# Kernel optimization log

Measured on AMD Instinct MI355X. Metric: run time of the kernel, lower is better.

The kernel has to match this reference:

```python
import jax, jax.numpy as jnp
import numpy as np

N_E, N_C, N_DL, N_IT, N_EP, N_HA, N_CA, N_AS = 11964, 188, 100, 7, 100, 10, 10, 7
D = 128
B, S = 256, 400
N_V = N_E + 1      # hypergraph vertices (exercises)
N_HE = N_C + 1     # hyperedges (concepts)
MEMB = 3           # concept memberships per exercise
BN_EPS = 1e-5


def _hg_v2v_mean(X, pair_v, pair_e):
    # HGNN+ smoothing: vertex -> hyperedge (mean) -> vertex (mean)
    ones_e = jnp.ones(pair_e.shape, X.dtype)
    e_deg = jnp.clip(jax.ops.segment_sum(ones_e, pair_e, num_segments=N_HE), 1.0)
    v_deg = jnp.clip(jax.ops.segment_sum(ones_e, pair_v, num_segments=N_V), 1.0)
    E = jax.ops.segment_sum(X[pair_v], pair_e, num_segments=N_HE) / e_deg[:, None]
    return jax.ops.segment_sum(E[pair_e], pair_v, num_segments=N_V) / v_deg[:, None]


def _hgnnp_conv(X, W, b, gamma, beta, mean, var, pair_v, pair_e, is_last):
    X = X @ W + b
    X = (X - mean) * jax.lax.rsqrt(var + BN_EPS) * gamma + beta  # eval-mode BN
    X = _hg_v2v_mean(X, pair_v, pair_e)
    if not is_last:
        X = jax.nn.relu(X)
    return X


def setup_inputs() -> dict:
    key = jax.random.key(0)
    ks = jax.random.split(key, 32)
    inp = {}
    inp['input_e'] = jax.random.randint(ks[0], (B, S), 0, N_V)
    inp['input_ed'] = jax.random.randint(ks[1], (B, S), 0, N_DL + 1)
    inp['input_ep'] = jax.random.randint(ks[2], (B, S), 0, N_EP + 1)
    inp['input_a'] = jax.random.randint(ks[3], (B, S), 0, 2)
    inp['input_as'] = jax.random.randint(ks[4], (B, S), 0, N_AS + 1)
    inp['input_ha'] = jax.random.randint(ks[5], (B, S), 0, N_HA + 1)
    inp['input_ca'] = jax.random.randint(ks[6], (B, S), 0, N_CA + 1)
    inp['input_it'] = jax.random.randint(ks[7], (B, S), 0, N_IT + 1)
    inp['deliver_h'] = jnp.zeros((B, D), jnp.float32)
    # hypergraph incidence (exercise-concept Q-matrix edges)
    rng = np.random.default_rng(0)
    inp['pair_v'] = jnp.asarray(np.repeat(np.arange(N_V), MEMB))
    inp['pair_e'] = jnp.asarray(rng.integers(0, N_HE, size=N_V * MEMB))
    inp['ec_map'] = jax.random.randint(ks[8], (N_V,), 0, N_HE)
    inp['ecd_map'] = jax.random.randint(ks[9], (N_V,), 0, N_DL + 1)
    # embedding tables (xavier-ish scale)
    def emb(k, n):
        return jax.random.normal(k, (n, D), jnp.float32) * 0.05
    inp['e_table'] = emb(ks[10], N_V)
    inp['c_table'] = emb(ks[11], N_HE)
    inp['ed_table'] = emb(ks[12], N_DL + 1)
    inp['cd_table'] = emb(ks[13], N_DL + 1)
    inp['a_table'] = emb(ks[14], 2)
    inp['it_table'] = emb(ks[15], N_IT + 1)
    inp['ep_table'] = emb(ks[16], N_EP + 1)
    inp['ha_table'] = emb(ks[17], N_HA + 1)
    inp['ca_table'] = emb(ks[18], N_CA + 1)
    inp['as_table'] = emb(ks[19], N_AS + 1)
    # HGNNP conv 1 & 2
    def lin(k, din, dout):
        return jax.random.normal(k, (din, dout), jnp.float32) * (1.0 / np.sqrt(din))
    inp['W1'] = lin(ks[20], D, D); inp['b1'] = jnp.zeros((D,), jnp.float32)
    inp['g1'] = jnp.ones((D,), jnp.float32); inp['be1'] = jnp.zeros((D,), jnp.float32)
    inp['m1'] = jnp.zeros((D,), jnp.float32); inp['v1'] = jnp.ones((D,), jnp.float32)
    inp['W2'] = lin(ks[21], D, D); inp['b2'] = jnp.zeros((D,), jnp.float32)
    inp['g2'] = jnp.ones((D,), jnp.float32); inp['be2'] = jnp.zeros((D,), jnp.float32)
    inp['m2'] = jnp.zeros((D,), jnp.float32); inp['v2'] = jnp.ones((D,), jnp.float32)
    # linear_i: (d_e + d_dl + d_ep + d_c + d_dl) -> d_x
    inp['Wi'] = lin(ks[22], 5 * D, D); inp['bi'] = jnp.zeros((D,), jnp.float32)
    # GRU knowledge-state cell: input = concat(x, a_emb) -> 2D, hidden D, 3 gates
    inp['Wg'] = lin(ks[23], 2 * D, 3 * D)
    inp['Ug'] = lin(ks[24], D, 3 * D)
    inp['bg'] = jnp.zeros((3 * D,), jnp.float32)
    # linear_predicting_e: d_x -> 1
    inp['We'] = lin(ks[25], D, 1); inp['beo'] = jnp.zeros((1,), jnp.float32)
    # linear_predicting_s: 4*d -> 1
    inp['Ws'] = lin(ks[26], 4 * D, 1); inp['bs'] = jnp.zeros((1,), jnp.float32)
    return inp


def reference(input_e, input_ed, input_ep, input_a, input_as, input_ha, input_ca, input_it,
              deliver_h, pair_v, pair_e, ec_map, ecd_map,
              e_table, c_table, ed_table, cd_table, a_table, it_table, ep_table,
              ha_table, ca_table, as_table,
              W1, b1, g1, be1, m1, v1, W2, b2, g2, be2, m2, v2,
              Wi, bi, Wg, Ug, bg, We, beo, Ws, bs):
    # 2-layer HGNN+ over the exercise hypergraph
    X = _hgnnp_conv(e_table, W1, b1, g1, be1, m1, v1, pair_v, pair_e, is_last=False)
    X = _hgnnp_conv(X, W2, b2, g2, be2, m2, v2, pair_v, pair_e, is_last=True)
    # embedding gathers  [B,S,D]
    e_emb = X[input_e]
    c_emb = c_table[ec_map[input_e]]
    cd_emb = cd_table[ecd_map[input_e]]
    ed_emb = ed_table[input_ed]
    ep_emb = ep_table[input_ep]
    x = jnp.tanh(jnp.concatenate([e_emb, ed_emb, ep_emb, c_emb, cd_emb], -1) @ Wi + bi)  # [B,S,D]
    a_emb = a_table[input_a]
    xs = jnp.moveaxis(jnp.concatenate([x, a_emb], -1), 1, 0)  # [S,B,2D]
    xp = jnp.moveaxis(x, 1, 0)                                # [S,B,D]

    def step(h, inputs):
        xin, xq = inputs
        y = jax.nn.sigmoid((h * xq) @ We + beo)[..., 0]  # predict from prior knowledge state
        gi = xin @ Wg + bg
        gh = h @ Ug
        iz, ir, inn = jnp.split(gi, 3, -1)
        hz, hr, hn = jnp.split(gh, 3, -1)
        z = jax.nn.sigmoid(iz + hz)
        r = jax.nn.sigmoid(ir + hr)
        n = jnp.tanh(inn + r * hn)
        return (1.0 - z) * n + z * h, y

    _, ys = jax.lax.scan(step, deliver_h, (xs, xp))
    pred_main = jnp.moveaxis(ys, 0, 1)  # [B,S]
    s_in = jnp.concatenate([ha_table[input_ha], ca_table[input_ca],
                            as_table[input_as], it_table[input_it]], -1)
    pred_s = jax.nn.sigmoid(s_in @ Ws + bs)[..., 0]  # [B,S]
    return pred_s, pred_main
```

## Files before the change

### kernel.cpp

```cpp
#include <hip/hip_runtime.h>

#define N_V   11965
#define N_HE  189
#define NPAIR 35895
#define BB    256
#define SS    400
#define DD    128
#define BSR   102400

typedef __bf16 bf16x8 __attribute__((ext_vector_type(8)));
typedef float  f32x4  __attribute__((ext_vector_type(4)));

__device__ __forceinline__ ushort f2bf(float f) {
    unsigned x = __float_as_uint(f);
    return (ushort)((x + 0x7FFFu + ((x >> 16) & 1u)) >> 16);
}
__device__ __forceinline__ float bf2f(ushort u) { return __uint_as_float(((unsigned)u) << 16); }
__device__ __forceinline__ float sigm(float x) { return 1.f / (1.f + __expf(-x)); }
__device__ __forceinline__ float tanh_f(float x) { return 2.f * sigm(2.f * x) - 1.f; }

struct P1Args {
    const int* pair_e;
    const float *b1, *g1, *be1, *m1, *v1;
    const float *b2, *g2, *be2, *m2, *v2;
    const float *W1, *W2, *Wi, *Wg;
    const float *ed_t, *ep_t, *c_t, *cd_t, *a_t, *bi, *bg;
    const float *ha_t, *ca_t, *as_t, *it_t, *Ws;
    int* e_deg;
    float* aff;
    ushort *W1T, *W2T, *WiTe, *WgT;
    float *edW, *epW, *cW, *cdW, *agi, *sd;
};

__global__ __launch_bounds__(384) void p1_kernel(P1Args A) {
    int bid = blockIdx.x, t = threadIdx.x;
    if (bid == 0) {
        if (t < 128) {
            float s = A.g1[t] * rsqrtf(A.v1[t] + 1e-5f);
            A.aff[t] = s;
            A.aff[128 + t] = A.b1[t] * s + A.be1[t] - A.m1[t] * s;
        } else if (t < 256) {
            int d = t - 128;
            float s = A.g2[d] * rsqrtf(A.v2[d] + 1e-5f);
            A.aff[256 + d] = s;
            A.aff[384 + d] = A.b2[d] * s + A.be2[d] - A.m2[d] * s;
        }
        return;
    }
    bid -= 1;
    if (bid < 94) {
        int p = bid * 384 + t;
        if (p < NPAIR) atomicAdd(&A.e_deg[A.pair_e[p]], 1);
        return;
    }
    bid -= 94;
    if (bid < 43) {
        int i = bid * 384 + t;
        if (i < 16384) { int k = i >> 7, n = i & 127; A.W1T[n * 128 + k] = f2bf(A.W1[i]); }
        return;
    }
    bid -= 43;
    if (bid < 43) {
        int i = bid * 384 + t;
        if (i < 16384) { int k = i >> 7, n = i & 127; A.W2T[n * 128 + k] = f2bf(A.W2[i]); }
        return;
    }
    bid -= 43;
    if (bid < 43) {
        int i = bid * 384 + t;
        if (i < 16384) { int k = i >> 7, n = i & 127; A.WiTe[n * 128 + k] = f2bf(A.Wi[i]); }
        return;
    }
    bid -= 43;
    if (bid < 128) {
        int i = bid * 384 + t;
        if (i < 49152) { int k = i / 384, n = i % 384; A.WgT[n * 128 + k] = f2bf(A.Wg[i]); }
        return;
    }
    bid -= 128;
    if (bid < 101) {
        if (t < 128) {
            float acc = 0.f;
            for (int k = 0; k < 128; ++k)
                acc += A.ed_t[bid * 128 + k] * A.Wi[(128 + k) * 128 + t];
            A.edW[bid * 128 + t] = acc + A.bi[t];
        }
        return;
    }
    bid -= 101;
    if (bid < 101) {
        if (t < 128) {
            float acc = 0.f;
            for (int k = 0; k < 128; ++k)
                acc += A.ep_t[bid * 128 + k] * A.Wi[(256 + k) * 128 + t];
            A.epW[bid * 128 + t] = acc;
        }
        return;
    }
    bid -= 101;
    if (bid < 189) {
        if (t < 128) {
            float acc = 0.f;
            for (int k = 0; k < 128; ++k)
                acc += A.c_t[bid * 128 + k] * A.Wi[(384 + k) * 128 + t];
            A.cW[bid * 128 + t] = acc;
        }
        return;
    }
    bid -= 189;
    if (bid < 101) {
        if (t < 128) {
            float acc = 0.f;
            for (int k = 0; k < 128; ++k)
                acc += A.cd_t[bid * 128 + k] * A.Wi[(512 + k) * 128 + t];
            A.cdW[bid * 128 + t] = acc;
        }
        return;
    }
    bid -= 101;
    if (bid < 2) {
        float acc = 0.f;
        for (int k = 0; k < 128; ++k)
            acc += A.a_t[bid * 128 + k] * A.Wg[(128 + k) * 384 + t];
        A.agi[bid * 384 + t] = acc + A.bg[t];
        return;
    }
    bid -= 2;
    {
        int r = bid;
        const float* tab; int woff, row;
        if (r < 11)      { tab = A.ha_t; row = r;      woff = 0;   }
        else if (r < 22) { tab = A.ca_t; row = r - 11; woff = 128; }
        else if (r < 30) { tab = A.as_t; row = r - 22; woff = 256; }
        else             { tab = A.it_t; row = r - 30; woff = 384; }
        if (t < 64) {
            float p = tab[row * 128 + t] * A.Ws[woff + t]
                    + tab[row * 128 + 64 + t] * A.Ws[woff + 64 + t];
            #pragma unroll
            for (int o = 32; o > 0; o >>= 1) p += __shfl_xor(p, o);
            if (t == 0) A.sd[r] = p;
        }
    }
}

__global__ void cvt_kernel(const float* __restrict__ src, ushort* __restrict__ dst, int n) {
    int i = blockIdx.x * 256 + threadIdx.x;
    if (i < n) dst[i] = f2bf(src[i]);
}

__global__ void csr_prefix(const int* __restrict__ e_deg, int* __restrict__ start) {
    __shared__ int sc[256];
    int t = threadIdx.x;
    int d = (t < N_HE) ? e_deg[t] : 0;
    sc[t] = d;
    __syncthreads();
    for (int off = 1; off < 256; off <<= 1) {
        int v = (t >= off) ? sc[t - off] : 0;
        __syncthreads();
        sc[t] += v;
        __syncthreads();
    }
    if (t < N_HE) start[t] = sc[t] - d;
    if (t == N_HE - 1) start[N_HE] = sc[t];
}

__global__ void csr_fill(const int* __restrict__ pair_e, const int* __restrict__ pair_v,
                         const int* __restrict__ start, int* __restrict__ cursor,
                         int* __restrict__ list) {
    int p = blockIdx.x * 384 + threadIdx.x;
    if (p >= NPAIR) return;
    int e = pair_e[p];
    int pos = atomicAdd(&cursor[e], 1);
    list[start[e] + pos] = pair_v[p];
}

template <int NT>
__global__ __launch_bounds__(256) void gemm_mfma(
    const ushort* __restrict__ Amat, const ushort* __restrict__ BT,
    float* __restrict__ out, int M,
    const float* __restrict__ colS, const float* __restrict__ colB,
    const float* __restrict__ agi, const int* __restrict__ aidx) {
    const int N = NT * 16;
    int lane = threadIdx.x & 63, wave = threadIdx.x >> 6;
    int q = lane >> 4, c = lane & 15;
    int rowbase = blockIdx.x * 64 + wave * 16;
    int arow = rowbase + c;
    if (arow > M - 1) arow = M - 1;
    f32x4 acc[NT];
#pragma unroll
    for (int i = 0; i < NT; ++i) acc[i] = (f32x4){0.f, 0.f, 0.f, 0.f};
#pragma unroll
    for (int ko = 0; ko < 4; ++ko) {
        bf16x8 af = *(const bf16x8*)(Amat + (size_t)arow * 128 + ko * 32 + q * 8);
#pragma unroll
        for (int nt = 0; nt < NT; ++nt) {
            bf16x8 bfr = *(const bf16x8*)(BT + (size_t)(nt * 16 + c) * 128 + ko * 32 + q * 8);
            acc[nt] = __builtin_amdgcn_mfma_f32_16x16x32_bf16(af, bfr, acc[nt], 0, 0, 0);
        }
    }
#pragma unroll
    for (int nt = 0; nt < NT; ++nt) {
        int col = nt * 16 + c;
        float s = colS ? colS[col] : 1.f;
        float bb = colB ? colB[col] : 0.f;
#pragma unroll
        for (int r = 0; r < 4; ++r) {
            int row = rowbase + q * 4 + r;
            if (row < M) {
                float v = acc[nt][r] * s + bb;
                if (agi) v += agi[aidx[row] * N + col];
                out[(size_t)row * N + col] = v;
            }
        }
    }
}

__global__ __launch_bounds__(512) void edge_mean(const float* __restrict__ Y,
                                                 const int* __restrict__ list,
                                                 const int* __restrict__ start,
                                                 float* __restrict__ E) {
    __shared__ float red[4][128];
    int e = blockIdx.x;
    int d = threadIdx.x & 127, g = threadIdx.x >> 7;
    int s0 = start[e], n = start[e + 1] - s0;
    float acc = 0.f;
    for (int i = g; i < n; i += 4) acc += Y[(size_t)list[s0 + i] * DD + d];
    red[g][d] = acc;
    __syncthreads();
    if (g == 0) {
        float v = red[0][d] + red[1][d] + red[2][d] + red[3][d];
        E[e * DD + d] = v / (float)(n > 0 ? n : 1);
    }
}

__global__ void v_mean(const float* __restrict__ E, const int* __restrict__ pair_e,
                       ushort* __restrict__ Xo, int relu) {
    int idx = blockIdx.x * 256 + threadIdx.x;
    if (idx >= N_V * DD) return;
    int v = idx >> 7, d = idx & 127;
    float a = E[pair_e[3 * v] * DD + d] + E[pair_e[3 * v + 1] * DD + d] +
              E[pair_e[3 * v + 2] * DD + d];
    a *= (1.f / 3.f);
    if (relu) a = fmaxf(a, 0.f);
    Xo[idx] = f2bf(a);
}

__global__ void k3_kernel(const int* __restrict__ in_e, const int* __restrict__ in_ed,
                          const int* __restrict__ in_ep, const float* __restrict__ XW,
                          const float* __restrict__ cW, const float* __restrict__ cdW,
                          const float* __restrict__ edW, const float* __restrict__ epW,
                          const int* __restrict__ ec_map, const int* __restrict__ ecd_map,
                          ushort* __restrict__ xbf) {
    int idx = blockIdx.x * 256 + threadIdx.x;
    if (idx >= BSR * DD) return;
    int row = idx >> 7, d = idx & 127;
    int e = in_e[row];
    float v = XW[(size_t)e * DD + d] + cW[ec_map[e] * DD + d] + cdW[ecd_map[e] * DD + d] +
              edW[in_ed[row] * DD + d] + epW[in_ep[row] * DD + d];
    xbf[idx] = f2bf(tanh_f(v));
}

__global__ void pred_s_kernel(const int* __restrict__ ha, const int* __restrict__ ca,
                              const int* __restrict__ as_, const int* __restrict__ it,
                              const float* __restrict__ sd, const float* __restrict__ bs,
                              float* __restrict__ out) {
    int i = blockIdx.x * 256 + threadIdx.x;
    if (i >= BSR) return;
    float v = sd[ha[i]] + sd[11 + ca[i]] + sd[22 + as_[i]] + sd[30 + it[i]] + bs[0];
    out[i] = sigm(v);
}

__global__ void
__attribute__((amdgpu_flat_work_group_size(768, 768), amdgpu_waves_per_eu(3, 3)))
gru_scan(
    const float* __restrict__ gi, const ushort* __restrict__ xb,
    const float* __restrict__ Ug, const float* __restrict__ h0,
    const float* __restrict__ We, const float* __restrict__ beo_p,
    float* __restrict__ out) {
    __shared__ __align__(16) float h_s[128];
    __shared__ float pp1[384];
    __shared__ float pp0h[128];
    __shared__ float n_sL[128];
    __shared__ float p_s[128];
    int b = blockIdx.x, t = threadIdx.x;
    int khalf = (t >= 384) ? 1 : 0;
    int n = t - 384 * khalf;
    float ugf[64];
    {
        const float* up = Ug + (size_t)(khalf * 64) * 384 + n;
#pragma unroll
        for (int j = 0; j < 64; ++j) ugf[j] = up[j * 384];
    }
#pragma unroll
    for (int j = 0; j < 64; ++j) asm volatile("" : "+v"(ugf[j]));
    float beo = beo_p[0];
    float wev = 0.f;
    if (t < 128) { wev = We[t]; h_s[t] = h0[b * 128 + t]; }
    const float* gip = gi + (size_t)b * SS * 384;
    const ushort* xp = xb + (size_t)b * SS * 128;
    float gz_nx = 0.f, gr_nx = 0.f, gn_nx = 0.f, xw_nx = 0.f;
    if (t < 128) {
        gz_nx = gip[t];
        xw_nx = bf2f(xp[t]) * wev;
    } else if (t >= 256 && t < 384) {
        gr_nx = gip[t - 128];
        gn_nx = gip[t];
    }
    float* omain = out + BSR + b * SS;
    __syncthreads();
    for (int s = 0; s < SS; ++s) {
        float gz = gz_nx, gr = gr_nx, gn = gn_nx, xw = xw_nx;
        if (s + 1 < SS) {
            const float* g2 = gip + (size_t)(s + 1) * 384;
            if (t < 128) {
                gz_nx = g2[t];
                xw_nx = bf2f(xp[(size_t)(s + 1) * 128 + t]) * wev;
            } else if (t >= 256 && t < 384) {
                gr_nx = g2[t - 128];
                gn_nx = g2[t];
            }
        }
        const float4* h4 = (const float4*)h_s + khalf * 16;
        float4 a4 = make_float4(0.f, 0.f, 0.f, 0.f);
#pragma unroll
        for (int j = 0; j < 16; ++j) {
            float4 hv = h4[j];
            a4.x = fmaf(hv.x, ugf[4 * j + 0], a4.x);
            a4.y = fmaf(hv.y, ugf[4 * j + 1], a4.y);
            a4.z = fmaf(hv.z, ugf[4 * j + 2], a4.z);
            a4.w = fmaf(hv.w, ugf[4 * j + 3], a4.w);
        }
        float part = (a4.x + a4.y) + (a4.z + a4.w);
        if (khalf) pp1[n] = part;
        else if (t >= 128 && t < 256) pp0h[t - 128] = part;
        __syncthreads();
        float z = 0.f, h_old = 0.f;
        if (t < 128) {
            float gh = part + pp1[t];
            z = sigm(gz + gh);
            h_old = h_s[t];
            p_s[t] = h_old * xw;
        } else if (t >= 256 && t < 384) {
            float ghn = part + pp1[t];
            float ghr = pp0h[t - 256] + pp1[t - 128];
            float r = sigm(gr + ghr);
            n_sL[t - 256] = tanh_f(gn + r * ghn);
        }
        __syncthreads();
        if (t < 128) {
            h_s[t] = (1.f - z) * n_sL[t] + z * h_old;
        } else if (t >= 384 && t < 448) {
            int l = t - 384;
            float pv = p_s[l] + p_s[l + 64];
#pragma unroll
            for (int o = 32; o > 0; o >>= 1) pv += __shfl_xor(pv, o);
            if (l == 0) omain[s] = sigm(pv + beo);
        }
        __syncthreads();
    }
}

extern "C" void kernel_launch(void* const* d_in, const int* in_sizes, int n_in,
                              void* d_out, int out_size, void* d_ws, size_t ws_size,
                              hipStream_t stream) {
    const int* in_e   = (const int*)d_in[0];
    const int* in_ed  = (const int*)d_in[1];
    const int* in_ep  = (const int*)d_in[2];
    const int* in_a   = (const int*)d_in[3];
    const int* in_as  = (const int*)d_in[4];
    const int* in_ha  = (const int*)d_in[5];
    const int* in_ca  = (const int*)d_in[6];
    const int* in_it  = (const int*)d_in[7];
    const float* deliver_h = (const float*)d_in[8];
    const int* pair_v = (const int*)d_in[9];
    const int* pair_e = (const int*)d_in[10];
    const int* ec_map = (const int*)d_in[11];
    const int* ecd_map= (const int*)d_in[12];
    const float* e_table  = (const float*)d_in[13];
    const float* c_table  = (const float*)d_in[14];
    const float* ed_table = (const float*)d_in[15];
    const float* cd_table = (const float*)d_in[16];
    const float* a_table  = (const float*)d_in[17];
    const float* it_table = (const float*)d_in[18];
    const float* ep_table = (const float*)d_in[19];
    const float* ha_table = (const float*)d_in[20];
    const float* ca_table = (const float*)d_in[21];
    const float* as_table = (const float*)d_in[22];
    const float* W1 = (const float*)d_in[23];
    const float* b1 = (const float*)d_in[24];
    const float* g1 = (const float*)d_in[25];
    const float* be1= (const float*)d_in[26];
    const float* m1 = (const float*)d_in[27];
    const float* v1 = (const float*)d_in[28];
    const float* W2 = (const float*)d_in[29];
    const float* b2 = (const float*)d_in[30];
    const float* g2 = (const float*)d_in[31];
    const float* be2= (const float*)d_in[32];
    const float* m2 = (const float*)d_in[33];
    const float* v2 = (const float*)d_in[34];
    const float* Wi = (const float*)d_in[35];
    const float* bi = (const float*)d_in[36];
    const float* Wg = (const float*)d_in[37];
    const float* Ug = (const float*)d_in[38];
    const float* bg = (const float*)d_in[39];
    const float* We = (const float*)d_in[40];
    const float* beo= (const float*)d_in[41];
    const float* Ws = (const float*)d_in[42];
    const float* bs = (const float*)d_in[43];
    float* out = (float*)d_out;
    char* ws = (char*)d_ws;

    size_t off = 0;
    auto alloc = [&](size_t bytes) { size_t o = off; off += (bytes + 255) & ~(size_t)255; return o; };
    size_t o_degcur = alloc(378 * 4);
    size_t o_start  = alloc(190 * 4);
    size_t o_list   = alloc((size_t)NPAIR * 4);
    size_t o_aff    = alloc(512 * 4);
    size_t o_W1T    = alloc(16384 * 2);
    size_t o_W2T    = alloc(16384 * 2);
    size_t o_WiTe   = alloc(16384 * 2);
    size_t o_WgT    = alloc(49152 * 2);
    size_t o_edW    = alloc(101 * 128 * 4);
    size_t o_epW    = alloc(101 * 128 * 4);
    size_t o_cW     = alloc(189 * 128 * 4);
    size_t o_cdW    = alloc(101 * 128 * 4);
    size_t o_agi    = alloc(2 * 384 * 4);
    size_t o_sd     = alloc(38 * 4);
    size_t o_etb    = alloc((size_t)N_V * DD * 2);
    size_t o_E      = alloc((size_t)N_HE * DD * 4);
    size_t o_Y      = alloc((size_t)N_V * DD * 4);
    size_t o_X1     = alloc((size_t)N_V * DD * 2);
    size_t o_X2     = alloc((size_t)N_V * DD * 2);
    size_t o_XW     = alloc((size_t)N_V * DD * 4);
    size_t o_xbf    = alloc((size_t)BSR * DD * 2);
    size_t o_gi     = alloc((size_t)BSR * 384 * 4);

    int*    e_deg  = (int*)(ws + o_degcur);
    int*    cursor = e_deg + 189;
    int*    startp = (int*)(ws + o_start);
    int*    listp  = (int*)(ws + o_list);
    float*  aff    = (float*)(ws + o_aff);
    ushort* W1T    = (ushort*)(ws + o_W1T);
    ushort* W2T    = (ushort*)(ws + o_W2T);
    ushort* WiTe   = (ushort*)(ws + o_WiTe);
    ushort* WgT    = (ushort*)(ws + o_WgT);
    float*  edW    = (float*)(ws + o_edW);
    float*  epW    = (float*)(ws + o_epW);
    float*  cW     = (float*)(ws + o_cW);
    float*  cdW    = (float*)(ws + o_cdW);
    float*  agi    = (float*)(ws + o_agi);
    float*  sd     = (float*)(ws + o_sd);
    ushort* e_tb   = (ushort*)(ws + o_etb);
    float*  E      = (float*)(ws + o_E);
    float*  Y      = (float*)(ws + o_Y);
    ushort* X1b    = (ushort*)(ws + o_X1);
    ushort* X2b    = (ushort*)(ws + o_X2);
    float*  XW     = (float*)(ws + o_XW);
    ushort* xbf    = (ushort*)(ws + o_xbf);
    float*  gi     = (float*)(ws + o_gi);

    hipMemsetAsync(ws + o_degcur, 0, 378 * 4, stream);

    P1Args pa;
    pa.pair_e = pair_e;
    pa.b1 = b1; pa.g1 = g1; pa.be1 = be1; pa.m1 = m1; pa.v1 = v1;
    pa.b2 = b2; pa.g2 = g2; pa.be2 = be2; pa.m2 = m2; pa.v2 = v2;
    pa.W1 = W1; pa.W2 = W2; pa.Wi = Wi; pa.Wg = Wg;
    pa.ed_t = ed_table; pa.ep_t = ep_table; pa.c_t = c_table; pa.cd_t = cd_table;
    pa.a_t = a_table; pa.bi = bi; pa.bg = bg;
    pa.ha_t = ha_table; pa.ca_t = ca_table; pa.as_t = as_table; pa.it_t = it_table; pa.Ws = Ws;
    pa.e_deg = e_deg; pa.aff = aff;
    pa.W1T = W1T; pa.W2T = W2T; pa.WiTe = WiTe; pa.WgT = WgT;
    pa.edW = edW; pa.epW = epW; pa.cW = cW; pa.cdW = cdW; pa.agi = agi; pa.sd = sd;
    p1_kernel<<<884, 384, 0, stream>>>(pa);

    cvt_kernel<<<(N_V * DD + 255) / 256, 256, 0, stream>>>(e_table, e_tb, N_V * DD);
    csr_prefix<<<1, 256, 0, stream>>>(e_deg, startp);
    csr_fill<<<94, 384, 0, stream>>>(pair_e, pair_v, startp, cursor, listp);

    pred_s_kernel<<<(BSR + 255) / 256, 256, 0, stream>>>(in_ha, in_ca, in_as, in_it, sd, bs, out);

    gemm_mfma<8><<<(N_V + 63) / 64, 256, 0, stream>>>(e_tb, W1T, Y, N_V, aff, aff + 128,
                                                      nullptr, nullptr);
    edge_mean<<<N_HE, 512, 0, stream>>>(Y, listp, startp, E);
    v_mean<<<(N_V * DD + 255) / 256, 256, 0, stream>>>(E, pair_e, X1b, 1);
    gemm_mfma<8><<<(N_V + 63) / 64, 256, 0, stream>>>(X1b, W2T, Y, N_V, aff + 256, aff + 384,
                                                      nullptr, nullptr);
    edge_mean<<<N_HE, 512, 0, stream>>>(Y, listp, startp, E);
    v_mean<<<(N_V * DD + 255) / 256, 256, 0, stream>>>(E, pair_e, X2b, 0);
    gemm_mfma<8><<<(N_V + 63) / 64, 256, 0, stream>>>(X2b, WiTe, XW, N_V, nullptr, nullptr,
                                                      nullptr, nullptr);
    k3_kernel<<<(BSR * DD + 255) / 256, 256, 0, stream>>>(in_e, in_ed, in_ep, XW, cW, cdW, edW,
                                                          epW, ec_map, ecd_map, xbf);
    gemm_mfma<24><<<BSR / 64, 256, 0, stream>>>(xbf, WgT, gi, BSR, nullptr, nullptr, agi, in_a);
    gru_scan<<<BB, 768, 0, stream>>>(gi, xbf, Ug, deliver_h, We, beo, out);
}
```

Measured before the change: 1.015 ms.

## Store GRU recurrent weights as packed bf16 registers and split K four ways

The recurrent matrix Ug is now converted to a transposed bf16 copy in the prep kernel. Each GRU-scan thread holds 32 packed registers covering two output columns over a quarter of K, where it previously held 64 fp32 registers for one column over half of K. Partial sums go to a 4x392 shared buffer and are reduced by the gate threads. This lowers register pressure and relaxes the waves-per-EU bound. The cost is bf16 rounding of Ug inside the recurrence, extra unpack work and more shared-memory reads in the reduction.

After: 1.011 ms. About the same (-0.4%).

```diff
diff --git a/kernel.cpp b/kernel.cpp
--- a/kernel.cpp
+++ b/kernel.cpp
@@ -18,17 +18,19 @@
 __device__ __forceinline__ float bf2f(ushort u) { return __uint_as_float(((unsigned)u) << 16); }
 __device__ __forceinline__ float sigm(float x) { return 1.f / (1.f + __expf(-x)); }
 __device__ __forceinline__ float tanh_f(float x) { return 2.f * sigm(2.f * x) - 1.f; }
+__device__ __forceinline__ float blo(unsigned u) { return __uint_as_float(u << 16); }
+__device__ __forceinline__ float bhi(unsigned u) { return __uint_as_float(u); }
 
 struct P1Args {
     const int* pair_e;
     const float *b1, *g1, *be1, *m1, *v1;
     const float *b2, *g2, *be2, *m2, *v2;
-    const float *W1, *W2, *Wi, *Wg;
+    const float *W1, *W2, *Wi, *Wg, *Ug;
     const float *ed_t, *ep_t, *c_t, *cd_t, *a_t, *bi, *bg;
     const float *ha_t, *ca_t, *as_t, *it_t, *Ws;
     int* e_deg;
     float* aff;
-    ushort *W1T, *W2T, *WiTe, *WgT;
+    ushort *W1T, *W2T, *WiTe, *WgT, *UgT;
     float *edW, *epW, *cW, *cdW, *agi, *sd;
 };
 
@@ -75,6 +77,12 @@
     if (bid < 128) {
         int i = bid * 384 + t;
         if (i < 49152) { int k = i / 384, n = i % 384; A.WgT[n * 128 + k] = f2bf(A.Wg[i]); }
+        return;
+    }
+    bid -= 128;
+    if (bid < 128) {
+        int i = bid * 384 + t;
+        if (i < 49152) { int k = i / 384, n = i % 384; A.UgT[n * 128 + k] = f2bf(A.Ug[i]); }
         return;
     }
     bid -= 128;
@@ -271,28 +279,27 @@
 }
 
 __global__ void
-__attribute__((amdgpu_flat_work_group_size(768, 768), amdgpu_waves_per_eu(3, 3)))
+__attribute__((amdgpu_flat_work_group_size(768, 768), amdgpu_waves_per_eu(2, 3)))
 gru_scan(
     const float* __restrict__ gi, const ushort* __restrict__ xb,
-    const float* __restrict__ Ug, const float* __restrict__ h0,
+    const ushort* __restrict__ UgT, const float* __restrict__ h0,
     const float* __restrict__ We, const float* __restrict__ beo_p,
     float* __restrict__ out) {
     __shared__ __align__(16) float h_s[128];
-    __shared__ float pp1[384];
-    __shared__ float pp0h[128];
+    __shared__ float pp[4][392];
     __shared__ float n_sL[128];
     __shared__ float p_s[128];
     int b = blockIdx.x, t = threadIdx.x;
-    int khalf = (t >= 384) ? 1 : 0;
-    int n = t - 384 * khalf;
-    float ugf[64];
-    {
-        const float* up = Ug + (size_t)(khalf * 64) * 384 + n;
-#pragma unroll
-        for (int j = 0; j < 64; ++j) ugf[j] = up[j * 384];
-    }
-#pragma unroll
-    for (int j = 0; j < 64; ++j) asm volatile("" : "+v"(ugf[j]));
+    int kq = t / 192;
+    int cp = t % 192;
+    const unsigned* WA = (const unsigned*)(UgT + (size_t)cp * 128 + kq * 32);
+    const unsigned* WB = (const unsigned*)(UgT + (size_t)(cp + 192) * 128 + kq * 32);
+    unsigned a0 = WA[0], a1 = WA[1], a2 = WA[2], a3 = WA[3], a4 = WA[4], a5 = WA[5],
+             a6 = WA[6], a7 = WA[7], a8 = WA[8], a9 = WA[9], a10 = WA[10], a11 = WA[11],
+             a12 = WA[12], a13 = WA[13], a14 = WA[14], a15 = WA[15];
+    unsigned c0 = WB[0], c1 = WB[1], c2 = WB[2], c3 = WB[3], c4 = WB[4], c5 = WB[5],
+             c6 = WB[6], c7 = WB[7], c8 = WB[8], c9 = WB[9], c10 = WB[10], c11 = WB[11],
+             c12 = WB[12], c13 = WB[13], c14 = WB[14], c15 = WB[15];
     float beo = beo_p[0];
     float wev = 0.f;
     if (t < 128) { wev = We[t]; h_s[t] = h0[b * 128 + t]; }
@@ -309,6 +316,12 @@
     float* omain = out + BSR + b * SS;
     __syncthreads();
     for (int s = 0; s < SS; ++s) {
+#define PIN(X) asm volatile("" : "+v"(X));
+        PIN(a0) PIN(a1) PIN(a2) PIN(a3) PIN(a4) PIN(a5) PIN(a6) PIN(a7)
+        PIN(a8) PIN(a9) PIN(a10) PIN(a11) PIN(a12) PIN(a13) PIN(a14) PIN(a15)
+        PIN(c0) PIN(c1) PIN(c2) PIN(c3) PIN(c4) PIN(c5) PIN(c6) PIN(c7)
+        PIN(c8) PIN(c9) PIN(c10) PIN(c11) PIN(c12) PIN(c13) PIN(c14) PIN(c15)
+#undef PIN
         float gz = gz_nx, gr = gr_nx, gn = gn_nx, xw = xw_nx;
         if (s + 1 < SS) {
             const float* g2 = gip + (size_t)(s + 1) * 384;
@@ -320,31 +333,33 @@
                 gn_nx = g2[t];
             }
         }
-        const float4* h4 = (const float4*)h_s + khalf * 16;
-        float4 a4 = make_float4(0.f, 0.f, 0.f, 0.f);
-#pragma unroll
-        for (int j = 0; j < 16; ++j) {
-            float4 hv = h4[j];
-            a4.x = fmaf(hv.x, ugf[4 * j + 0], a4.x);
-            a4.y = fmaf(hv.y, ugf[4 * j + 1], a4.y);
-            a4.z = fmaf(hv.z, ugf[4 * j + 2], a4.z);
-            a4.w = fmaf(hv.w, ugf[4 * j + 3], a4.w);
-        }
-        float part = (a4.x + a4.y) + (a4.z + a4.w);
-        if (khalf) pp1[n] = part;
-        else if (t >= 128 && t < 256) pp0h[t - 128] = part;
+        const float4* h4 = (const float4*)h_s + kq * 8;
+        float accA = 0.f, accB = 0.f;
+#define FB(I, UL, UH, VL, VH) { float4 hv = h4[I]; \
+        accA = fmaf(hv.x, blo(UL), accA); accA = fmaf(hv.y, bhi(UL), accA); \
+        accA = fmaf(hv.z, blo(UH), accA); accA = fmaf(hv.w, bhi(UH), accA); \
+        accB = fmaf(hv.x, blo(VL), accB); accB = fmaf(hv.y, bhi(VL), accB); \
+        accB = fmaf(hv.z, blo(VH), accB); accB = fmaf(hv.w, bhi(VH), accB); }
+        FB(0, a0, a1, c0, c1)    FB(1, a2, a3, c2, c3)
+        FB(2, a4, a5, c4, c5)    FB(3, a6, a7, c6, c7)
+        FB(4, a8, a9, c8, c9)    FB(5, a10, a11, c10, c11)
+        FB(6, a12, a13, c12, c13) FB(7, a14, a15, c14, c15)
+#undef FB
+        pp[kq][cp] = accA;
+        pp[kq][cp + 192] = accB;
         __syncthreads();
         float z = 0.f, h_old = 0.f;
         if (t < 128) {
-            float gh = part + pp1[t];
-            z = sigm(gz + gh);
+            float S = pp[0][t] + pp[1][t] + pp[2][t] + pp[3][t];
+            z = sigm(gz + S);
             h_old = h_s[t];
             p_s[t] = h_old * xw;
         } else if (t >= 256 && t < 384) {
-            float ghn = part + pp1[t];
-            float ghr = pp0h[t - 256] + pp1[t - 128];
-            float r = sigm(gr + ghr);
-            n_sL[t - 256] = tanh_f(gn + r * ghn);
+            int j = t - 256;
+            float Sr = pp[0][128 + j] + pp[1][128 + j] + pp[2][128 + j] + pp[3][128 + j];
+            float Sn = pp[0][256 + j] + pp[1][256 + j] + pp[2][256 + j] + pp[3][256 + j];
+            float r = sigm(gr + Sr);
+            n_sL[j] = tanh_f(gn + r * Sn);
         }
         __syncthreads();
         if (t < 128) {
@@ -420,6 +435,7 @@
     size_t o_W2T    = alloc(16384 * 2);
     size_t o_WiTe   = alloc(16384 * 2);
     size_t o_WgT    = alloc(49152 * 2);
+    size_t o_UgT    = alloc(49152 * 2);
     size_t o_edW    = alloc(101 * 128 * 4);
     size_t o_epW    = alloc(101 * 128 * 4);
     size_t o_cW     = alloc(189 * 128 * 4);
@@ -444,6 +460,7 @@
     ushort* W2T    = (ushort*)(ws + o_W2T);
     ushort* WiTe   = (ushort*)(ws + o_WiTe);
     ushort* WgT    = (ushort*)(ws + o_WgT);
+    ushort* UgTp   = (ushort*)(ws + o_UgT);
     float*  edW    = (float*)(ws + o_edW);
     float*  epW    = (float*)(ws + o_epW);
     float*  cW     = (float*)(ws + o_cW);
@@ -465,14 +482,14 @@
     pa.pair_e = pair_e;
     pa.b1 = b1; pa.g1 = g1; pa.be1 = be1; pa.m1 = m1; pa.v1 = v1;
     pa.b2 = b2; pa.g2 = g2; pa.be2 = be2; pa.m2 = m2; pa.v2 = v2;
-    pa.W1 = W1; pa.W2 = W2; pa.Wi = Wi; pa.Wg = Wg;
+    pa.W1 = W1; pa.W2 = W2; pa.Wi = Wi; pa.Wg = Wg; pa.Ug = Ug;
     pa.ed_t = ed_table; pa.ep_t = ep_table; pa.c_t = c_table; pa.cd_t = cd_table;
     pa.a_t = a_table; pa.bi = bi; pa.bg = bg;
     pa.ha_t = ha_table; pa.ca_t = ca_table; pa.as_t = as_table; pa.it_t = it_table; pa.Ws = Ws;
     pa.e_deg = e_deg; pa.aff = aff;
-    pa.W1T = W1T; pa.W2T = W2T; pa.WiTe = WiTe; pa.WgT = WgT;
+    pa.W1T = W1T; pa.W2T = W2T; pa.WiTe = WiTe; pa.WgT = WgT; pa.UgT = UgTp;
     pa.edW = edW; pa.epW = epW; pa.cW = cW; pa.cdW = cdW; pa.agi = agi; pa.sd = sd;
-    p1_kernel<<<884, 384, 0, stream>>>(pa);
+    p1_kernel<<<1012, 384, 0, stream>>>(pa);
 
     cvt_kernel<<<(N_V * DD + 255) / 256, 256, 0, stream>>>(e_table, e_tb, N_V * DD);
     csr_prefix<<<1, 256, 0, stream>>>(e_deg, startp);
@@ -493,5 +510,5 @@
     k3_kernel<<<(BSR * DD + 255) / 256, 256, 0, stream>>>(in_e, in_ed, in_ep, XW, cW, cdW, edW,
                                                           epW, ec_map, ecd_map, xbf);
     gemm_mfma<24><<<BSR / 64, 256, 0, stream>>>(xbf, WgT, gi, BSR, nullptr, nullptr, agi, in_a);
-    gru_scan<<<BB, 768, 0, stream>>>(gi, xbf, Ug, deliver_h, We, beo, out);
-}
+    gru_scan<<<BB, 768, 0, stream>>>(gi, xbf, UgTp, deliver_h, We, beo, out);
+}
```
